# Optimization experiments

Hardware: AMD Instinct MI355X
Metric: run time of the kernel (lower is better)

The kernel has to match this reference:

```python
import jax, jax.numpy as jnp
import numpy as np

B, N, D_IN, D_OUT = 2, 2048, 2048, 2048
H, G = 16, 4            # num_heads, n_kv_groups
HD = D_OUT // H         # head_dim = 128
REP = H // G            # query heads per kv head = 4


def setup_inputs() -> dict:
    key = jax.random.key(0)
    ks = jax.random.split(key, 6)
    s = lambda fan_in: 1.0 / np.sqrt(fan_in)
    return {
        "x": jax.random.normal(ks[0], (B, N, D_IN), jnp.float32),
        "Wq": jax.random.normal(ks[1], (D_IN, D_OUT), jnp.float32) * s(D_IN),
        "Wk": jax.random.normal(ks[2], (D_IN, G * HD), jnp.float32) * s(D_IN),
        "Wv": jax.random.normal(ks[3], (D_IN, G * HD), jnp.float32) * s(D_IN),
        "Wo": jax.random.normal(ks[4], (D_OUT, D_OUT), jnp.float32) * s(D_OUT),
        "bo": jnp.zeros((D_OUT,), jnp.float32),
    }


def reference(x, Wq, Wk, Wv, Wo, bo):
    b, n, _ = x.shape
    # projections
    q = (x @ Wq).reshape(b, n, G, REP, HD)   # query heads grouped: h = g*REP + r
    k = (x @ Wk).reshape(b, n, G, HD)
    v = (x @ Wv).reshape(b, n, G, HD)
    # grouped attention scores; KV broadcast over REP instead of repeat_kv
    scores = jnp.einsum('bqgrd,bkgd->bgrqk', q, k)  # [b,G,REP,N,N]
    causal = jnp.tril(jnp.ones((n, n), bool))       # allowed positions
    scores = jnp.where(causal, scores, -jnp.inf)
    w = jax.nn.softmax(scores / np.float32(np.sqrt(HD)), axis=-1)
    ctx = jnp.einsum('bgrqk,bkgd->bqgrd', w, v).reshape(b, n, D_OUT)
    return ctx @ Wo + bo
```

## Files before the change

kernel.cpp:

```cpp
#include <hip/hip_runtime.h>
#include <stdint.h>

typedef __attribute__((ext_vector_type(8))) __bf16 bf16x8;
typedef __attribute__((ext_vector_type(4))) float f32x4;
typedef __attribute__((ext_vector_type(4))) short short4v;

static constexpr int SEQ  = 2048;
static constexpr int DQKV = 3072;
static constexpr int HD   = 128;

__device__ __forceinline__ short f2bf(float f) {
  unsigned u = __builtin_bit_cast(unsigned, f);
  u += 0x7fffu + ((u >> 16) & 1u);
  return (short)(u >> 16);
}

__device__ __forceinline__ unsigned pack2(float a, float b) {
  return (unsigned)(unsigned short)f2bf(a) | ((unsigned)(unsigned short)f2bf(b) << 16);
}

__device__ __forceinline__ void gl_lds16(const void* g, void* l) {
  __builtin_amdgcn_global_load_lds(
      (const __attribute__((address_space(1))) void*)g,
      (__attribute__((address_space(3))) void*)l, 16, 0, 0);
}

__global__ __launch_bounds__(256)
void prep_kernel(const float* __restrict__ x, const float* __restrict__ Wq,
                 const float* __restrict__ Wk, const float* __restrict__ Wv,
                 const float* __restrict__ Wo,
                 short* __restrict__ xb, short* __restrict__ WqkvT,
                 short* __restrict__ WoT) {
  int blk = blockIdx.x, tid = threadIdx.x;
  if (blk < 8192) {
    int i = blk * 256 + tid;
    float4 v = reinterpret_cast<const float4*>(x)[i];
    short4v o;
    o[0] = f2bf(v.x); o[1] = f2bf(v.y); o[2] = f2bf(v.z); o[3] = f2bf(v.w);
    *reinterpret_cast<short4v*>(xb + (size_t)i * 4) = o;
    return;
  }
  blk -= 8192;
  __shared__ float tile[32][33];
  const float* in; short* out; int C, bx, by;
  if (blk < 4096)      { in = Wq; out = WqkvT;                     C = 2048; bx = blk & 63; by = blk >> 6; }
  else if (blk < 5120) { int t = blk - 4096; in = Wk; out = WqkvT + (size_t)2048 * 2048; C = 512; bx = t & 15; by = t >> 4; }
  else if (blk < 6144) { int t = blk - 5120; in = Wv; out = WqkvT + (size_t)2560 * 2048; C = 512; bx = t & 15; by = t >> 4; }
  else                 { int t = blk - 6144; in = Wo; out = WoT;   C = 2048; bx = t & 63; by = t >> 6; }
  const int R = 2048;
  int c0 = bx * 32, r0 = by * 32, tx = tid & 31, ty = tid >> 5;
  for (int i = 0; i < 4; i++)
    tile[ty + i * 8][tx] = in[(size_t)(r0 + ty + i * 8) * C + c0 + tx];
  __syncthreads();
  for (int i = 0; i < 4; i++)
    out[(size_t)(c0 + ty + i * 8) * R + r0 + tx] = f2bf(tile[tx][ty + i * 8]);
}

__global__ __launch_bounds__(256) void transpose_v_kernel(const short* __restrict__ qkv,
                                                          short* __restrict__ vT) {
  __shared__ short tile[32][33];
  int n0 = blockIdx.x * 32, c0 = blockIdx.y * 32, b = blockIdx.z;
  int tx = threadIdx.x & 31, ty = threadIdx.x >> 5;
  for (int i = 0; i < 4; i++)
    tile[ty + i * 8][tx] = qkv[(size_t)(b * SEQ + n0 + ty + i * 8) * DQKV + 2560 + c0 + tx];
  __syncthreads();
  for (int i = 0; i < 4; i++)
    vT[(size_t)(b * 512 + c0 + ty + i * 8) * SEQ + n0 + tx] = tile[tx][ty + i * 8];
}

template <int F32OUT>
__global__ __launch_bounds__(256)
void gemm_bt_kernel(const short* __restrict__ A, const short* __restrict__ BT,
                    void* __restrict__ Cout, const float* __restrict__ bias,
                    int M, int N, int K, int qcols, float qscale) {
  __shared__ __align__(16) short As[4096];
  __shared__ __align__(16) short Bs[4096];
  const int tid = threadIdx.x, lane = tid & 63, w = tid >> 6;
  const int l15 = lane & 15, quad = lane >> 4, q8 = quad * 8;
  const int row0 = blockIdx.y * 128, col0 = blockIdx.x * 128;
  const int wm = (w >> 1) * 64, wn = (w & 1) * 64;
  f32x4 acc[4][4] = {};
  const short* ga0 = A  + (size_t)(row0 + w * 16 + (lane >> 2)) * K + (lane & 3) * 8;
  const short* gb0 = BT + (size_t)(col0 + w * 16 + (lane >> 2)) * K + (lane & 3) * 8;
  for (int kt = 0; kt < K; kt += 32) {
    gl_lds16(ga0 + kt,                   As + w * 512);
    gl_lds16(ga0 + (size_t)64 * K + kt,  As + 2048 + w * 512);
    gl_lds16(gb0 + kt,                   Bs + w * 512);
    gl_lds16(gb0 + (size_t)64 * K + kt,  Bs + 2048 + w * 512);
    __syncthreads();
    bf16x8 af[4], bfr[4];
    for (int i = 0; i < 4; i++)
      af[i] = *reinterpret_cast<const bf16x8*>(As + (wm + i * 16 + l15) * 32 + q8);
    for (int j = 0; j < 4; j++)
      bfr[j] = *reinterpret_cast<const bf16x8*>(Bs + (wn + j * 16 + l15) * 32 + q8);
    for (int i = 0; i < 4; i++)
      for (int j = 0; j < 4; j++)
        acc[i][j] = __builtin_amdgcn_mfma_f32_16x16x32_bf16(af[i], bfr[j], acc[i][j], 0, 0, 0);
    __syncthreads();
  }
  if (F32OUT) {
    float* C = (float*)Cout;
    for (int j = 0; j < 4; j++) {
      int col = col0 + wn + j * 16 + l15;
      float bv = bias[col];
      for (int i = 0; i < 4; i++)
        for (int r = 0; r < 4; r++)
          C[(size_t)(row0 + wm + i * 16 + quad * 4 + r) * N + col] = acc[i][j][r] + bv;
    }
  } else {
    short* C = (short*)Cout;
    for (int j = 0; j < 4; j++) {
      int col = col0 + wn + j * 16 + l15;
      float sc = (col < qcols) ? qscale : 1.0f;
      for (int i = 0; i < 4; i++)
        for (int r = 0; r < 4; r++)
          C[(size_t)(row0 + wm + i * 16 + quad * 4 + r) * N + col] = f2bf(acc[i][j][r] * sc);
    }
  }
}

__global__ __launch_bounds__(256, 2)
void attn_kernel(const short* __restrict__ qkv, const short* __restrict__ vT,
                 short* __restrict__ ctx) {
  __shared__ __align__(16) short Ks[16384];
  __shared__ __align__(16) short Vs[16384];
  __shared__ __align__(16) short Ps[4608];
  const int tid = threadIdx.x, lane = tid & 63, w = tid >> 6;
  const int l15 = lane & 15, quad = lane >> 4, q8 = quad * 8;
  const int idx = blockIdx.x;
  const int qt = 31 - (idx >> 5);
  const int h = (idx >> 1) & 15, b = idx & 1, g = h >> 2;

  bf16x8 qf[4];
  {
    const short* gq = qkv + (size_t)(b * SEQ + qt * 64 + w * 16 + l15) * DQKV + h * HD + q8;
    for (int ds = 0; ds < 4; ds++)
      qf[ds] = *reinterpret_cast<const bf16x8*>(gq + ds * 32);
  }
  bf16x8 ones;
  for (int i = 0; i < 8; i++) ones[i] = __builtin_bit_cast(__bf16, (short)0x3F80);

  f32x4 acco[8] = {};
  f32x4 accl = {};

  auto stage = [&](int buf, int kt) {
    const short* gk = qkv + (size_t)(b * SEQ + kt * 64 + w * 16 + (lane >> 2)) * DQKV +
                      2048 + g * HD + (lane & 3) * 8;
    for (int ks = 0; ks < 4; ks++)
      gl_lds16(gk + ks * 32, Ks + buf * 8192 + ks * 2048 + w * 512);
    for (int c = 0; c < 2; c++)
      for (int ih = 0; ih < 2; ih++)
        gl_lds16(vT + (size_t)(b * 512 + g * HD + ih * 64 + w * 16 + (lane >> 2)) * SEQ +
                     kt * 64 + c * 32 + (lane & 3) * 8,
                 Vs + buf * 8192 + c * 4096 + ih * 2048 + w * 512);
  };

  stage(0, 0);
  for (int kt = 0; kt <= qt; kt++) {
    const int cur = kt & 1;
    __syncthreads();
    if (kt < qt) stage(cur ^ 1, kt + 1);

    const short* Kb = Ks + cur * 8192;
    const short* Vb = Vs + cur * 8192;

    f32x4 accs[4] = {};
    for (int ds = 0; ds < 4; ds++)
      for (int j = 0; j < 4; j++) {
        bf16x8 kf = *reinterpret_cast<const bf16x8*>(Kb + ds * 2048 + (j * 16 + l15) * 32 + q8);
        accs[j] = __builtin_amdgcn_mfma_f32_16x16x32_bf16(kf, qf[ds], accs[j], 0, 0, 0);
      }

    if (kt == qt) {
      const int q = w * 16 + l15;
      for (int j = 0; j < 4; j++)
        for (int r = 0; r < 4; r++)
          if (j * 16 + quad * 4 + r > q) accs[j][r] = -1e38f;
    }

    for (int j = 0; j < 4; j++) {
      float p0 = exp2f(accs[j][0]), p1 = exp2f(accs[j][1]);
      float p2 = exp2f(accs[j][2]), p3 = exp2f(accs[j][3]);
      unsigned u0 = __builtin_bit_cast(unsigned, p0), u1 = __builtin_bit_cast(unsigned, p1);
      unsigned u2 = __builtin_bit_cast(unsigned, p2), u3 = __builtin_bit_cast(unsigned, p3);
      uint2 dd = make_uint2((u0 >> 16) | (u1 & 0xffff0000u),
                            (u2 >> 16) | (u3 & 0xffff0000u));
      *reinterpret_cast<uint2*>(Ps + w * 1152 + l15 * 72 + j * 16 + quad * 4) = dd;
    }
    asm volatile("s_waitcnt lgkmcnt(0)" ::: "memory");

    for (int c = 0; c < 2; c++) {
      bf16x8 pf = *reinterpret_cast<const bf16x8*>(Ps + w * 1152 + l15 * 72 + c * 32 + q8);
      accl = __builtin_amdgcn_mfma_f32_16x16x32_bf16(ones, pf, accl, 0, 0, 0);
      for (int nt = 0; nt < 8; nt++) {
        bf16x8 vf = *reinterpret_cast<const bf16x8*>(Vb + c * 4096 + (nt * 16 + l15) * 32 + q8);
        acco[nt] = __builtin_amdgcn_mfma_f32_16x16x32_bf16(vf, pf, acco[nt], 0, 0, 0);
      }
    }
  }

  const float invl = 1.f / accl[0];
  const size_t row = (size_t)(b * SEQ + qt * 64 + w * 16 + l15);
  for (int nt = 0; nt < 8; nt++) {
    uint2 dd = make_uint2(pack2(acco[nt][0] * invl, acco[nt][1] * invl),
                          pack2(acco[nt][2] * invl, acco[nt][3] * invl));
    *reinterpret_cast<uint2*>(ctx + row * 2048 + h * HD + nt * 16 + quad * 4) = dd;
  }
}

extern "C" void kernel_launch(void* const* d_in, const int* in_sizes, int n_in,
                              void* d_out, int out_size, void* d_ws, size_t ws_size,
                              hipStream_t stream) {
  const float* x  = (const float*)d_in[0];
  const float* Wq = (const float*)d_in[1];
  const float* Wk = (const float*)d_in[2];
  const float* Wv = (const float*)d_in[3];
  const float* Wo = (const float*)d_in[4];
  const float* bo = (const float*)d_in[5];
  float* out = (float*)d_out;

  const float sc2 = 0.08838834764831845f * 1.4426950408889634f;

  short* xb    = (short*)d_ws;
  short* WqkvT = xb    + (size_t)4096 * 2048;
  short* WoT   = WqkvT + (size_t)3072 * 2048;
  short* qkv   = WoT   + (size_t)2048 * 2048;
  short* vT    = qkv   + (size_t)4096 * 3072;
  short* ctx   = vT    + (size_t)1024 * 2048;

  prep_kernel<<<dim3(18432), dim3(256), 0, stream>>>(x, Wq, Wk, Wv, Wo, xb, WqkvT, WoT);
  gemm_bt_kernel<0><<<dim3(24, 32), dim3(256), 0, stream>>>(xb, WqkvT, qkv, nullptr,
                                                            4096, 3072, 2048, 2048, sc2);
  transpose_v_kernel<<<dim3(64, 16, 2), dim3(256), 0, stream>>>(qkv, vT);
  attn_kernel<<<dim3(1024), dim3(256), 0, stream>>>(qkv, vT, ctx);
  gemm_bt_kernel<1><<<dim3(16, 32), dim3(256), 0, stream>>>(ctx, WoT, out, bo,
                                                            4096, 2048, 2048, 0, 1.0f);
}
```

Before: 305.6 us.

## Enlarge attention query tile to 128 rows, deepen GEMM K-step, swizzle P tile

The attention kernel now runs 512 threads (8 waves) per block and covers 128 query rows, so each K/V tile staged into LDS is reused by twice as many queries. K and V loading is split between the two halves of the waves, and the causal mask is applied to the last two key tiles. The P scratch buffer uses an XOR swizzle instead of padding to avoid LDS bank conflicts. The GEMM loads 64 K-columns per barrier pair, halving the number of syncs, at the cost of more LDS per block and possibly lower occupancy.

```diff
diff --git a/kernel.cpp b/kernel.cpp
--- a/kernel.cpp
+++ b/kernel.cpp
@@ -73,8 +73,8 @@
 void gemm_bt_kernel(const short* __restrict__ A, const short* __restrict__ BT,
                     void* __restrict__ Cout, const float* __restrict__ bias,
                     int M, int N, int K, int qcols, float qscale) {
-  __shared__ __align__(16) short As[4096];
-  __shared__ __align__(16) short Bs[4096];
+  __shared__ __align__(16) short As[8192];
+  __shared__ __align__(16) short Bs[8192];
   const int tid = threadIdx.x, lane = tid & 63, w = tid >> 6;
   const int l15 = lane & 15, quad = lane >> 4, q8 = quad * 8;
   const int row0 = blockIdx.y * 128, col0 = blockIdx.x * 128;
@@ -82,20 +82,24 @@
   f32x4 acc[4][4] = {};
   const short* ga0 = A  + (size_t)(row0 + w * 16 + (lane >> 2)) * K + (lane & 3) * 8;
   const short* gb0 = BT + (size_t)(col0 + w * 16 + (lane >> 2)) * K + (lane & 3) * 8;
-  for (int kt = 0; kt < K; kt += 32) {
-    gl_lds16(ga0 + kt,                   As + w * 512);
-    gl_lds16(ga0 + (size_t)64 * K + kt,  As + 2048 + w * 512);
-    gl_lds16(gb0 + kt,                   Bs + w * 512);
-    gl_lds16(gb0 + (size_t)64 * K + kt,  Bs + 2048 + w * 512);
+  for (int kt = 0; kt < K; kt += 64) {
+    for (int s = 0; s < 2; s++) {
+      gl_lds16(ga0 + kt + s * 32,                  As + s * 4096 + w * 512);
+      gl_lds16(ga0 + (size_t)64 * K + kt + s * 32, As + s * 4096 + 2048 + w * 512);
+      gl_lds16(gb0 + kt + s * 32,                  Bs + s * 4096 + w * 512);
+      gl_lds16(gb0 + (size_t)64 * K + kt + s * 32, Bs + s * 4096 + 2048 + w * 512);
+    }
     __syncthreads();
-    bf16x8 af[4], bfr[4];
-    for (int i = 0; i < 4; i++)
-      af[i] = *reinterpret_cast<const bf16x8*>(As + (wm + i * 16 + l15) * 32 + q8);
-    for (int j = 0; j < 4; j++)
-      bfr[j] = *reinterpret_cast<const bf16x8*>(Bs + (wn + j * 16 + l15) * 32 + q8);
-    for (int i = 0; i < 4; i++)
+    for (int s = 0; s < 2; s++) {
+      bf16x8 af[4], bfr[4];
+      for (int i = 0; i < 4; i++)
+        af[i] = *reinterpret_cast<const bf16x8*>(As + s * 4096 + (wm + i * 16 + l15) * 32 + q8);
       for (int j = 0; j < 4; j++)
-        acc[i][j] = __builtin_amdgcn_mfma_f32_16x16x32_bf16(af[i], bfr[j], acc[i][j], 0, 0, 0);
+        bfr[j] = *reinterpret_cast<const bf16x8*>(Bs + s * 4096 + (wn + j * 16 + l15) * 32 + q8);
+      for (int i = 0; i < 4; i++)
+        for (int j = 0; j < 4; j++)
+          acc[i][j] = __builtin_amdgcn_mfma_f32_16x16x32_bf16(af[i], bfr[j], acc[i][j], 0, 0, 0);
+    }
     __syncthreads();
   }
   if (F32OUT) {
@@ -119,21 +123,21 @@
   }
 }
 
-__global__ __launch_bounds__(256, 2)
+__global__ __launch_bounds__(512, 4)
 void attn_kernel(const short* __restrict__ qkv, const short* __restrict__ vT,
                  short* __restrict__ ctx) {
   __shared__ __align__(16) short Ks[16384];
   __shared__ __align__(16) short Vs[16384];
-  __shared__ __align__(16) short Ps[4608];
+  __shared__ __align__(16) short Ps[8192];
   const int tid = threadIdx.x, lane = tid & 63, w = tid >> 6;
   const int l15 = lane & 15, quad = lane >> 4, q8 = quad * 8;
   const int idx = blockIdx.x;
-  const int qt = 31 - (idx >> 5);
+  const int qt = 15 - (idx >> 5);
   const int h = (idx >> 1) & 15, b = idx & 1, g = h >> 2;
 
   bf16x8 qf[4];
   {
-    const short* gq = qkv + (size_t)(b * SEQ + qt * 64 + w * 16 + l15) * DQKV + h * HD + q8;
+    const short* gq = qkv + (size_t)(b * SEQ + qt * 128 + w * 16 + l15) * DQKV + h * HD + q8;
     for (int ds = 0; ds < 4; ds++)
       qf[ds] = *reinterpret_cast<const bf16x8*>(gq + ds * 32);
   }
@@ -144,22 +148,27 @@
   f32x4 accl = {};
 
   auto stage = [&](int buf, int kt) {
-    const short* gk = qkv + (size_t)(b * SEQ + kt * 64 + w * 16 + (lane >> 2)) * DQKV +
-                      2048 + g * HD + (lane & 3) * 8;
-    for (int ks = 0; ks < 4; ks++)
-      gl_lds16(gk + ks * 32, Ks + buf * 8192 + ks * 2048 + w * 512);
-    for (int c = 0; c < 2; c++)
-      for (int ih = 0; ih < 2; ih++)
-        gl_lds16(vT + (size_t)(b * 512 + g * HD + ih * 64 + w * 16 + (lane >> 2)) * SEQ +
-                     kt * 64 + c * 32 + (lane & 3) * 8,
-                 Vs + buf * 8192 + c * 4096 + ih * 2048 + w * 512);
+    if (w < 4) {
+      const short* gk = qkv + (size_t)(b * SEQ + kt * 64 + w * 16 + (lane >> 2)) * DQKV +
+                        2048 + g * HD + (lane & 3) * 8;
+      for (int ks = 0; ks < 4; ks++)
+        gl_lds16(gk + ks * 32, Ks + buf * 8192 + ks * 2048 + w * 512);
+    } else {
+      const int w4 = w - 4;
+      for (int c = 0; c < 2; c++)
+        for (int ih = 0; ih < 2; ih++)
+          gl_lds16(vT + (size_t)(b * 512 + g * HD + ih * 64 + w4 * 16 + (lane >> 2)) * SEQ +
+                       kt * 64 + c * 32 + (lane & 3) * 8,
+                   Vs + buf * 8192 + c * 4096 + ih * 2048 + w4 * 512);
+    }
   };
 
+  const int kmax = 2 * qt + 1;
   stage(0, 0);
-  for (int kt = 0; kt <= qt; kt++) {
+  for (int kt = 0; kt <= kmax; kt++) {
     const int cur = kt & 1;
     __syncthreads();
-    if (kt < qt) stage(cur ^ 1, kt + 1);
+    if (kt < kmax) stage(cur ^ 1, kt + 1);
 
     const short* Kb = Ks + cur * 8192;
     const short* Vb = Vs + cur * 8192;
@@ -171,11 +180,11 @@
         accs[j] = __builtin_amdgcn_mfma_f32_16x16x32_bf16(kf, qf[ds], accs[j], 0, 0, 0);
       }
 
-    if (kt == qt) {
-      const int q = w * 16 + l15;
+    if (kt >= 2 * qt) {
+      const int qm = qt * 128 + w * 16 + l15 - kt * 64;
       for (int j = 0; j < 4; j++)
         for (int r = 0; r < 4; r++)
-          if (j * 16 + quad * 4 + r > q) accs[j][r] = -1e38f;
+          if (j * 16 + quad * 4 + r > qm) accs[j][r] = -1e38f;
     }
 
     for (int j = 0; j < 4; j++) {
@@ -185,12 +194,14 @@
       unsigned u2 = __builtin_bit_cast(unsigned, p2), u3 = __builtin_bit_cast(unsigned, p3);
       uint2 dd = make_uint2((u0 >> 16) | (u1 & 0xffff0000u),
                             (u2 >> 16) | (u3 & 0xffff0000u));
-      *reinterpret_cast<uint2*>(Ps + w * 1152 + l15 * 72 + j * 16 + quad * 4) = dd;
+      const int chw = (2 * j + (quad >> 1)) ^ (l15 & 7);
+      *reinterpret_cast<uint2*>(Ps + w * 1024 + l15 * 64 + chw * 8 + (quad & 1) * 4) = dd;
     }
     asm volatile("s_waitcnt lgkmcnt(0)" ::: "memory");
 
     for (int c = 0; c < 2; c++) {
-      bf16x8 pf = *reinterpret_cast<const bf16x8*>(Ps + w * 1152 + l15 * 72 + c * 32 + q8);
+      const int chr = (4 * c + quad) ^ (l15 & 7);
+      bf16x8 pf = *reinterpret_cast<const bf16x8*>(Ps + w * 1024 + l15 * 64 + chr * 8);
       accl = __builtin_amdgcn_mfma_f32_16x16x32_bf16(ones, pf, accl, 0, 0, 0);
       for (int nt = 0; nt < 8; nt++) {
         bf16x8 vf = *reinterpret_cast<const bf16x8*>(Vb + c * 4096 + (nt * 16 + l15) * 32 + q8);
@@ -200,7 +211,7 @@
   }
 
   const float invl = 1.f / accl[0];
-  const size_t row = (size_t)(b * SEQ + qt * 64 + w * 16 + l15);
+  const size_t row = (size_t)(b * SEQ + qt * 128 + w * 16 + l15);
   for (int nt = 0; nt < 8; nt++) {
     uint2 dd = make_uint2(pack2(acco[nt][0] * invl, acco[nt][1] * invl),
                           pack2(acco[nt][2] * invl, acco[nt][3] * invl));
@@ -232,7 +243,7 @@
   gemm_bt_kernel<0><<<dim3(24, 32), dim3(256), 0, stream>>>(xb, WqkvT, qkv, nullptr,
                                                             4096, 3072, 2048, 2048, sc2);
   transpose_v_kernel<<<dim3(64, 16, 2), dim3(256), 0, stream>>>(qkv, vT);
-  attn_kernel<<<dim3(1024), dim3(256), 0, stream>>>(qkv, vT, ctx);
+  attn_kernel<<<dim3(512), dim3(512), 0, stream>>>(qkv, vT, ctx);
   gemm_bt_kernel<1><<<dim3(16, 32), dim3(256), 0, stream>>>(ctx, WoT, out, bo,
                                                             4096, 2048, 2048, 0, 1.0f);
 }
```

Result: no change. 306.1 us (+0.1%).
